# Performance work log

Measured on AMD Instinct MI355X. Metric: run time of the kernel, lower is better.

## Reference

```python
import jax, jax.numpy as jnp
import numpy as np

EMB_DIM = 1024
HEAD_SIZE = 128
B, T = 8, 2048


def setup_inputs() -> dict:
    key = jax.random.key(0)
    kx, kk, kq, kv = jax.random.split(key, 4)
    x = jax.random.normal(kx, (B, T, EMB_DIM), dtype=jnp.float32)
    # torch nn.Linear(emb_dim, head_size, bias=False): weight [head_size, emb_dim], y = x @ W.T
    # store transposed as [emb_dim, head_size] for direct matmul
    s = 1.0 / np.sqrt(EMB_DIM)
    Wk = jax.random.uniform(kk, (EMB_DIM, HEAD_SIZE), dtype=jnp.float32, minval=-s, maxval=s)
    Wq = jax.random.uniform(kq, (EMB_DIM, HEAD_SIZE), dtype=jnp.float32, minval=-s, maxval=s)
    Wv = jax.random.uniform(kv, (EMB_DIM, HEAD_SIZE), dtype=jnp.float32, minval=-s, maxval=s)
    return {"x": x, "Wk": Wk, "Wq": Wq, "Wv": Wv}


def reference(x, Wk, Wq, Wv):
    Bb, Tt, C = x.shape
    k = jnp.einsum('btc,ch->bth', x, Wk)
    q = jnp.einsum('btc,ch->bth', x, Wq)
    v = jnp.einsum('btc,ch->bth', x, Wv)
    # NOTE: original computes k @ q^T (not q @ k^T) and scales by C**-0.5 (C = emb_dim)
    wei = jnp.einsum('bih,bjh->bij', k, q) * (C ** -0.5)  # [B, T, T]
    causal = jnp.tril(jnp.ones((Tt, Tt), dtype=bool))
    wei = jnp.where(causal, wei, -jnp.inf)
    wei = jax.nn.softmax(wei, axis=-1)
    out = jnp.einsum('bij,bjh->bih', wei, v)  # [B, T, head_size]
    return out
```

## Files before the change

kernel.cpp:

```cpp
#include <hip/hip_runtime.h>
#include <hip/hip_bf16.h>
#include <stdint.h>

#define Bn 8
#define Tn 2048
#define Cn 1024
#define Hn 128

typedef __attribute__((ext_vector_type(8))) short short8;
typedef __attribute__((ext_vector_type(4))) short short4v;
typedef __attribute__((ext_vector_type(4))) float f32x4;
typedef __attribute__((ext_vector_type(4))) int int4v;

static __device__ __forceinline__ unsigned short f2bf(float f) {
    union { float f; unsigned int u; } v; v.f = f;
    return (unsigned short)((v.u + 0x7FFFu + ((v.u >> 16) & 1u)) >> 16);
}
static __device__ __forceinline__ float bf2f(unsigned short h) {
    union { unsigned int u; float f; } v; v.u = ((unsigned int)h) << 16;
    return v.f;
}

static __device__ __forceinline__ short8 cvt8(f32x4 a, f32x4 b) {
    union { unsigned int u[4]; short8 s; } r;
    asm("v_cvt_pk_bf16_f32 %0, %1, %2" : "=v"(r.u[0]) : "v"(a[0]), "v"(a[1]));
    asm("v_cvt_pk_bf16_f32 %0, %1, %2" : "=v"(r.u[1]) : "v"(a[2]), "v"(a[3]));
    asm("v_cvt_pk_bf16_f32 %0, %1, %2" : "=v"(r.u[2]) : "v"(b[0]), "v"(b[1]));
    asm("v_cvt_pk_bf16_f32 %0, %1, %2" : "=v"(r.u[3]) : "v"(b[2]), "v"(b[3]));
    return r.s;
}

static __device__ __forceinline__ void async16(const void* g, void* l) {
    __builtin_amdgcn_global_load_lds(
        (const __attribute__((address_space(1))) unsigned int*)g,
        (__attribute__((address_space(3))) unsigned int*)l,
        16, 0, 0);
}

#define KSCALE 0.04508422f

#define BASE_BYTES (3u * Bn * Tn * Hn * 2u + 3u * Hn * Cn * 2u)
#define SLOT_SH 2080
#define NBLK_FA 576
#define UPB_FA 72
#define CCHUNK 8

__global__ __launch_bounds__(256) void wt_prep(const float* __restrict__ Wk,
                                               const float* __restrict__ Wq,
                                               const float* __restrict__ Wv,
                                               unsigned short* __restrict__ WT) {
    int z = blockIdx.y;
    const float* W = (z == 0) ? Wk : (z == 1) ? Wq : Wv;
    unsigned short* wt = WT + (size_t)z * Hn * Cn;
    int o = blockIdx.x * 256 + threadIdx.x;
    int d = o >> 10;
    int k = o & (Cn - 1);
    wt[o] = f2bf(W[k * Hn + d]);
}

__global__ __launch_bounds__(512) void proj10(const float* __restrict__ x,
                                              const unsigned short* __restrict__ WTb,
                                              unsigned short* __restrict__ Kb,
                                              unsigned short* __restrict__ Qb,
                                              unsigned short* __restrict__ VT) {
    __shared__ __align__(16) unsigned short Bsm[2][384 * 64];
    __shared__ __align__(16) float Asm[2][64 * 64];
    int tid = threadIdx.x;
    int lane = tid & 63, w = tid >> 6;
    int lr = lane & 15, lg = lane >> 4;
    int wm = w >> 2, wn = w & 3;

    int u = ((int)(blockIdx.x & 7)) * 32 + ((int)blockIdx.x >> 3);
    int r0 = u * 64;

    const unsigned short* bsrcp[6];
    #pragma unroll
    for (int i = 0; i < 6; ++i) {
        int brow = (w * 6 + i) * 8 + (lane >> 3);
        int bslot = (lane & 7) ^ (brow & 7);
        bsrcp[i] = WTb + (size_t)brow * Cn + bslot * 8;
    }
    const float* asrcp[2];
    #pragma unroll
    for (int i = 0; i < 2; ++i) {
        int arow = (w * 2 + i) * 4 + (lane >> 4);
        int aslot = (lane & 15) ^ (arow & 7);
        asrcp[i] = x + (size_t)(r0 + arow) * Cn + aslot * 4;
    }

    auto STAGE = [&](int bb, int k0) {
        #pragma unroll
        for (int i = 0; i < 6; ++i)
            async16(bsrcp[i] + k0, &Bsm[bb][(w * 6 + i) * 512]);
        #pragma unroll
        for (int i = 0; i < 2; ++i)
            async16(asrcp[i] + k0, &Asm[bb][(w * 2 + i) * 256]);
    };

    f32x4 acc[2][6] = {};
    STAGE(0, 0);
    __syncthreads();
    int cur = 0;
    for (int ks = 0; ks < 16; ++ks) {
        if (ks < 15) STAGE(cur ^ 1, (ks + 1) * 64);
        const char* ab = (const char*)&Asm[cur][0];
        const char* bbp = (const char*)&Bsm[cur][0];
        #pragma unroll
        for (int kk = 0; kk < 2; ++kk) {
            short8 af[2], bf[6];
            #pragma unroll
            for (int m = 0; m < 2; ++m) {
                int row = wm * 32 + m * 16 + lr;
                const char* abase = ab + row * 256;
                f32x4 a0 = *(const f32x4*)(abase + (((kk * 8 + lg * 2)     ^ (row & 7)) << 4));
                f32x4 a1 = *(const f32x4*)(abase + (((kk * 8 + lg * 2 + 1) ^ (row & 7)) << 4));
                af[m] = cvt8(a0, a1);
            }
            #pragma unroll
            for (int c = 0; c < 6; ++c) {
                int row = wn * 96 + c * 16 + lr;
                bf[c] = *(const short8*)(bbp + row * 128 + (((kk * 4 + lg) ^ (row & 7)) << 4));
            }
            #pragma unroll
            for (int m = 0; m < 2; ++m)
                #pragma unroll
                for (int c = 0; c < 6; ++c)
                    acc[m][c] = __builtin_amdgcn_mfma_f32_16x16x32_bf16(af[m], bf[c], acc[m][c], 0, 0, 0);
        }
        __syncthreads();
        cur ^= 1;
    }

    int bb = r0 >> 11;
    int tb = r0 & 2047;
    #pragma unroll
    for (int m = 0; m < 2; ++m)
        #pragma unroll
        for (int c = 0; c < 6; ++c) {
            int col0 = wn * 96 + c * 16;
            int z = col0 >> 7;
            int d = (col0 & 127) + lr;
            if (z == 2) {
                int t = tb + wm * 32 + m * 16 + lg * 4;
                short4v pv;
                pv[0] = (short)f2bf(acc[m][c][0]);
                pv[1] = (short)f2bf(acc[m][c][1]);
                pv[2] = (short)f2bf(acc[m][c][2]);
                pv[3] = (short)f2bf(acc[m][c][3]);
                *(short4v*)(VT + ((size_t)(bb * Hn + d) << 11) + t) = pv;
            } else {
                unsigned short* outp = (z == 0) ? Kb : Qb;
                float sc = (z == 0) ? KSCALE : 1.0f;
                #pragma unroll
                for (int r = 0; r < 4; ++r) {
                    int i = r0 + wm * 32 + m * 16 + lg * 4 + r;
                    outp[(size_t)i * Hn + d] = f2bf(acc[m][c][r] * sc);
                }
            }
        }
}

__global__ __launch_bounds__(512) void fattn8(const unsigned short* __restrict__ Kb,
                                              const unsigned short* __restrict__ Qb,
                                              const unsigned short* __restrict__ VT,
                                              unsigned short* __restrict__ accP) {
    __shared__ __align__(16) unsigned short Ksm[2][32 * 128];
    __shared__ __align__(16) unsigned short Vsm[2][128 * 32];
    __shared__ __align__(16) unsigned short pbuf[8][16][48];
    int tid = threadIdx.x, lane = tid & 63, w = tid >> 6;
    int lr = lane & 15, lg = lane >> 4;

    int cpx = gridDim.x >> 3;
    int u = ((int)blockIdx.x & 7) * cpx + ((int)blockIdx.x >> 3);
    int b = u / UPB_FA, rem = u - b * UPB_FA;
    int g = 0, p = 0;
    for (;;) {
        int P = (4 * g + 4 + CCHUNK - 1) / CCHUNK;
        if (rem < P) { p = rem; break; }
        rem -= P; ++g;
    }
    int nt = 4 * g + 4;
    int P = (nt + CCHUNK - 1) / CCHUNK;
    int q = nt / P, r = nt % P;
    int begin = p * q + (p < r ? p : r);
    int size = q + (p < r ? 1 : 0);

    int i0 = g * 128 + w * 16;
    int tmax = (i0 + 15) >> 5;
    const unsigned short* kb = Kb + (size_t)b * Tn * Hn;
    const unsigned short* qb = Qb + (size_t)b * Tn * Hn;
    const unsigned short* vt = VT + (size_t)b * Hn * Tn;

    short8 kf[4];
    #pragma unroll
    for (int kk = 0; kk < 4; ++kk)
        kf[kk] = *(const short8*)(kb + (size_t)(i0 + lr) * Hn + kk * 32 + lg * 8);

    int krow = tid >> 4, kcol = (tid & 15) * 8;
    int vrow = tid >> 2, vcol = (tid & 3) * 8;
    int4v kreg, vreg;
    auto LOADT = [&](int tt) {
        int j0 = tt * 32;
        kreg = *(const int4v*)(qb + (size_t)(j0 + krow) * Hn + kcol);
        vreg = *(const int4v*)(vt + (size_t)vrow * Tn + j0 + vcol);
    };
    auto WRITET = [&](int bb) {
        *(int4v*)((char*)&Ksm[bb][0] + krow * 256 + ((kcol * 2) ^ ((krow & 7) << 4))) = kreg;
        *(int4v*)((char*)&Vsm[bb][0] + vrow * 64 + vcol * 2) = vreg;
    };

    f32x4 acc[8] = {};
    float ssum[4] = {0.f, 0.f, 0.f, 0.f};

    LOADT(begin);
    WRITET(0);
    __syncthreads();
    int cur = 0;
    for (int ti = 0; ti < size; ++ti) {
        int tt = begin + ti;
        if (ti + 1 < size) LOADT(tt + 1);
        if (tt <= tmax) {
            int j0 = tt * 32;
            const char* kbp = (const char*)&Ksm[cur][0];
            const char* vbp = (const char*)&Vsm[cur][0];
            f32x4 sa0 = {}, sa1 = {};
            #pragma unroll
            for (int kk = 0; kk < 4; ++kk) {
                int row = lr;
                short8 qf = *(const short8*)(kbp + row * 256 + (((kk * 64) + lg * 16) ^ ((row & 7) << 4)));
                sa0 = __builtin_amdgcn_mfma_f32_16x16x32_bf16(kf[kk], qf, sa0, 0, 0, 0);
            }
            #pragma unroll
            for (int kk = 0; kk < 4; ++kk) {
                int row = 16 + lr;
                short8 qf = *(const short8*)(kbp + row * 256 + (((kk * 64) + lg * 16) ^ ((row & 7) << 4)));
                sa1 = __builtin_amdgcn_mfma_f32_16x16x32_bf16(kf[kk], qf, sa1, 0, 0, 0);
            }
            bool needmask = (j0 + 31 > i0);
            #pragma unroll
            for (int rr = 0; rr < 4; ++rr) {
                float v0 = sa0[rr], v1 = sa1[rr];
                if (needmask) {
                    int i = i0 + lg * 4 + rr;
                    if (j0 + lr > i)      v0 = -1e30f;
                    if (j0 + 16 + lr > i) v1 = -1e30f;
                }
                float p0 = __builtin_amdgcn_exp2f(v0);
                float p1 = __builtin_amdgcn_exp2f(v1);
                ssum[rr] += p0 + p1;
                pbuf[w][lg * 4 + rr][lr] = f2bf(p0);
                pbuf[w][lg * 4 + rr][16 + lr] = f2bf(p1);
            }
            short8 pf = *(const short8*)(&pbuf[w][lr][lg * 8]);
            #pragma unroll
            for (int n = 0; n < 8; ++n) {
                int row = n * 16 + lr;
                short8 vf = *(const short8*)(vbp + row * 64 + lg * 16);
                acc[n] = __builtin_amdgcn_mfma_f32_16x16x32_bf16(pf, vf, acc[n], 0, 0, 0);
            }
        }
        if (ti + 1 < size) WRITET(cur ^ 1);
        __syncthreads();
        cur ^= 1;
    }

    unsigned short* dst = accP + (size_t)u * 8 * SLOT_SH + (size_t)w * SLOT_SH;
    #pragma unroll
    for (int n = 0; n < 8; ++n) {
        short4v pv;
        pv[0] = (short)f2bf(acc[n][0]);
        pv[1] = (short)f2bf(acc[n][1]);
        pv[2] = (short)f2bf(acc[n][2]);
        pv[3] = (short)f2bf(acc[n][3]);
        *(short4v*)(dst + n * 256 + lane * 4) = pv;
    }
    #pragma unroll
    for (int rr = 0; rr < 4; ++rr) {
        float s = ssum[rr];
        s += __shfl_xor(s, 1);
        s += __shfl_xor(s, 2);
        s += __shfl_xor(s, 4);
        s += __shfl_xor(s, 8);
        if (lr == 0) ((float*)(dst + 2048))[lg * 4 + rr] = s;
    }
}

__global__ __launch_bounds__(256) void combine3(const unsigned short* __restrict__ accP,
                                                float* __restrict__ out) {
    int cpx = gridDim.x >> 3;
    int bidx = ((int)blockIdx.x & 7) * cpx + ((int)blockIdx.x >> 3);
    int b = bidx >> 7, tile = bidx & 127;
    int g = tile >> 3, wq = tile & 7;
    int ub = b * UPB_FA;
    for (int gg = 0; gg < g; ++gg) ub += (4 * gg + 4 + CCHUNK - 1) / CCHUNK;
    int nt = 4 * g + 4;
    int P = (nt + CCHUNK - 1) / CCHUNK;

    int tid = threadIdx.x;
    int row = tid >> 4;
    int c8 = (tid & 15) * 8;

    const unsigned short* base = accP + ((size_t)ub * 8 + wq) * SLOT_SH;
    const size_t pstr = (size_t)8 * SLOT_SH;
    float den = 0.f;
    for (int pp = 0; pp < P; ++pp) den += ((const float*)(base + pp * pstr + 2048))[row];
    float inv = 1.0f / den;

    int lgg = row >> 2, r4 = row & 3;
    float ov[8];
    #pragma unroll
    for (int cc = 0; cc < 8; ++cc) {
        int col = c8 + cc;
        int n = col >> 4, lrr = col & 15;
        int flat = n * 256 + (lgg * 16 + lrr) * 4 + r4;
        float s = 0.f;
        for (int pp = 0; pp < P; ++pp) s += bf2f(base[pp * pstr + flat]);
        ov[cc] = s * inv;
    }
    float* op = out + ((size_t)(b * Tn + tile * 16 + row)) * Hn + c8;
    *(f32x4*)op       = f32x4{ov[0], ov[1], ov[2], ov[3]};
    *(f32x4*)(op + 4) = f32x4{ov[4], ov[5], ov[6], ov[7]};
}

__global__ __launch_bounds__(256) void attn(const unsigned short* __restrict__ Kb,
                                            const unsigned short* __restrict__ Qb,
                                            const unsigned short* __restrict__ VT,
                                            float* __restrict__ out) {
    __shared__ unsigned short pbuf[4][16][32];
    __shared__ __align__(16) float accbuf[4][16][132];
    __shared__ float ssbuf[4][16];
    int lane = threadIdx.x & 63;
    int w = threadIdx.x >> 6;
    int b = blockIdx.y;
    int xb = blockIdx.x;
    int tile = (xb & 1) ? (127 - (xb >> 1)) : (xb >> 1);
    int i0 = tile * 16;
    int lr = lane & 15, lg = lane >> 4;

    const unsigned short* kb = Kb + (size_t)b * Tn * Hn;
    const unsigned short* qb = Qb + (size_t)b * Tn * Hn;
    const unsigned short* vt = VT + (size_t)b * Hn * Tn;

    short8 kf[4];
    #pragma unroll
    for (int kk = 0; kk < 4; ++kk)
        kf[kk] = *(const short8*)(kb + (size_t)(i0 + lr) * Hn + kk * 32 + lg * 8);

    f32x4 acc[8] = {};
    float ssum[4] = {0.f, 0.f, 0.f, 0.f};

    int nt = (i0 + 15) / 32 + 1;
    for (int tt = w; tt < nt; tt += 4) {
        int j0 = tt * 32;
        f32x4 sa0 = {}, sa1 = {};
        #pragma unroll
        for (int kk = 0; kk < 4; ++kk) {
            short8 q0 = *(const short8*)(qb + (size_t)(j0 + lr) * Hn + kk * 32 + lg * 8);
            sa0 = __builtin_amdgcn_mfma_f32_16x16x32_bf16(kf[kk], q0, sa0, 0, 0, 0);
        }
        #pragma unroll
        for (int kk = 0; kk < 4; ++kk) {
            short8 q1 = *(const short8*)(qb + (size_t)(j0 + 16 + lr) * Hn + kk * 32 + lg * 8);
            sa1 = __builtin_amdgcn_mfma_f32_16x16x32_bf16(kf[kk], q1, sa1, 0, 0, 0);
        }
        bool needmask = (j0 + 31 > i0);
        #pragma unroll
        for (int r = 0; r < 4; ++r) {
            float v0 = sa0[r], v1 = sa1[r];
            if (needmask) {
                int i = i0 + lg * 4 + r;
                if (j0 + lr > i)      v0 = -1e30f;
                if (j0 + 16 + lr > i) v1 = -1e30f;
            }
            float p0 = __builtin_amdgcn_exp2f(v0);
            float p1 = __builtin_amdgcn_exp2f(v1);
            ssum[r] += p0 + p1;
            pbuf[w][lg * 4 + r][lr] = f2bf(p0);
            pbuf[w][lg * 4 + r][16 + lr] = f2bf(p1);
        }
        short8 pf = *(const short8*)(&pbuf[w][lr][lg * 8]);
        #pragma unroll
        for (int n = 0; n < 8; ++n) {
            short8 vf = *(const short8*)(vt + (size_t)(n * 16 + lr) * Tn + j0 + lg * 8);
            acc[n] = __builtin_amdgcn_mfma_f32_16x16x32_bf16(pf, vf, acc[n], 0, 0, 0);
        }
    }

    #pragma unroll
    for (int r = 0; r < 4; ++r) {
        float s = ssum[r];
        s += __shfl_xor(s, 1);
        s += __shfl_xor(s, 2);
        s += __shfl_xor(s, 4);
        s += __shfl_xor(s, 8);
        if (lr == 0) ssbuf[w][lg * 4 + r] = s;
    }
    #pragma unroll
    for (int n = 0; n < 8; ++n)
        #pragma unroll
        for (int r = 0; r < 4; ++r)
            accbuf[w][lg * 4 + r][n * 16 + lr] = acc[n][r];
    __syncthreads();

    int row = threadIdx.x >> 5;
    int col = (threadIdx.x & 31) * 4;
    #pragma unroll
    for (int h = 0; h < 2; ++h) {
        int rr = row + h * 8;
        f32x4 s = *(const f32x4*)(&accbuf[0][rr][col]);
        #pragma unroll
        for (int ww = 1; ww < 4; ++ww) {
            f32x4 t = *(const f32x4*)(&accbuf[ww][rr][col]);
            s[0] += t[0]; s[1] += t[1]; s[2] += t[2]; s[3] += t[3];
        }
        float den = ssbuf[0][rr] + ssbuf[1][rr] + ssbuf[2][rr] + ssbuf[3][rr];
        float inv = 1.0f / den;
        s[0] *= inv; s[1] *= inv; s[2] *= inv; s[3] *= inv;
        *(f32x4*)(&out[((size_t)(b * Tn + i0 + rr)) * Hn + col]) = s;
    }
}

extern "C" void kernel_launch(void* const* d_in, const int* in_sizes, int n_in,
                              void* d_out, int out_size, void* d_ws, size_t ws_size,
                              hipStream_t stream) {
    const float* x  = (const float*)d_in[0];
    const float* Wk = (const float*)d_in[1];
    const float* Wq = (const float*)d_in[2];
    const float* Wv = (const float*)d_in[3];

    unsigned short* Kb = (unsigned short*)d_ws;
    unsigned short* Qb = Kb + (size_t)Bn * Tn * Hn;
    unsigned short* VT = Qb + (size_t)Bn * Tn * Hn;
    unsigned short* WT = VT + (size_t)Bn * Tn * Hn;
    unsigned short* accP = (unsigned short*)((char*)d_ws + BASE_BYTES);

    wt_prep<<<dim3(512, 3), 256, 0, stream>>>(Wk, Wq, Wv, WT);
    proj10<<<dim3(256), 512, 0, stream>>>(x, WT, Kb, Qb, VT);

    const size_t need = (size_t)BASE_BYTES + (size_t)NBLK_FA * 8 * SLOT_SH * 2;
    if (ws_size >= need) {
        fattn8<<<dim3(NBLK_FA), 512, 0, stream>>>(Kb, Qb, VT, accP);
        combine3<<<dim3(1024), 256, 0, stream>>>(accP, (float*)d_out);
    } else {
        attn<<<dim3(128, 8), 256, 0, stream>>>(Kb, Qb, VT, (float*)d_out);
    }
}
```

Measured before the change: 85.87 us.

## Load projection A operand directly to registers with triple-buffered weight staging

The QKV projection kernel no longer stages the fp32 x tile through shared memory. Each lane loads its A fragment straight from global memory into double-buffered registers one step ahead. Weight tiles use a 3-deep shared-memory ring with a k-step of 32, and the loop waits on vmcnt counts instead of full syncthreads, with setprio around the MFMA block. This cuts LDS traffic and the shared-memory footprint and deepens prefetch, but it relies on hand-tuned waitcnt values and on uncoalesced direct global loads of x.

```diff
diff --git a/kernel.cpp b/kernel.cpp
--- a/kernel.cpp
+++ b/kernel.cpp
@@ -58,13 +58,12 @@
     wt[o] = f2bf(W[k * Hn + d]);
 }
 
-__global__ __launch_bounds__(512) void proj10(const float* __restrict__ x,
+__global__ __launch_bounds__(512) void proj11(const float* __restrict__ x,
                                               const unsigned short* __restrict__ WTb,
                                               unsigned short* __restrict__ Kb,
                                               unsigned short* __restrict__ Qb,
                                               unsigned short* __restrict__ VT) {
-    __shared__ __align__(16) unsigned short Bsm[2][384 * 64];
-    __shared__ __align__(16) float Asm[2][64 * 64];
+    __shared__ __align__(16) unsigned short Bsm[3][384 * 32];
     int tid = threadIdx.x;
     int lane = tid & 63, w = tid >> 6;
     int lr = lane & 15, lg = lane >> 4;
@@ -73,62 +72,70 @@
     int u = ((int)(blockIdx.x & 7)) * 32 + ((int)blockIdx.x >> 3);
     int r0 = u * 64;
 
-    const unsigned short* bsrcp[6];
-    #pragma unroll
-    for (int i = 0; i < 6; ++i) {
-        int brow = (w * 6 + i) * 8 + (lane >> 3);
-        int bslot = (lane & 7) ^ (brow & 7);
-        bsrcp[i] = WTb + (size_t)brow * Cn + bslot * 8;
-    }
-    const float* asrcp[2];
-    #pragma unroll
-    for (int i = 0; i < 2; ++i) {
-        int arow = (w * 2 + i) * 4 + (lane >> 4);
-        int aslot = (lane & 15) ^ (arow & 7);
-        asrcp[i] = x + (size_t)(r0 + arow) * Cn + aslot * 4;
-    }
-
+    const unsigned short* bsrc[3];
+    #pragma unroll
+    for (int i = 0; i < 3; ++i) {
+        int brow = (w * 3 + i) * 16 + (lane >> 2);
+        int bslot = (lane & 3) ^ ((brow >> 1) & 3);
+        bsrc[i] = WTb + (size_t)brow * Cn + bslot * 8;
+    }
     auto STAGE = [&](int bb, int k0) {
         #pragma unroll
-        for (int i = 0; i < 6; ++i)
-            async16(bsrcp[i] + k0, &Bsm[bb][(w * 6 + i) * 512]);
-        #pragma unroll
-        for (int i = 0; i < 2; ++i)
-            async16(asrcp[i] + k0, &Asm[bb][(w * 2 + i) * 256]);
+        for (int i = 0; i < 3; ++i)
+            async16(bsrc[i] + k0, &Bsm[bb][(w * 3 + i) * 512]);
     };
 
+    const float* aq0 = x + (size_t)(r0 + wm * 32 + lr) * Cn + lg * 8;
+    const float* aq1 = aq0 + 16 * Cn;
+    auto LOADA = [&](f32x4 (&d)[4], int k0) {
+        d[0] = *(const f32x4*)(aq0 + k0);
+        d[1] = *(const f32x4*)(aq0 + k0 + 4);
+        d[2] = *(const f32x4*)(aq1 + k0);
+        d[3] = *(const f32x4*)(aq1 + k0 + 4);
+    };
+
     f32x4 acc[2][6] = {};
+    f32x4 A0[4], A1[4];
+    int rbuf = 0;
+
     STAGE(0, 0);
-    __syncthreads();
-    int cur = 0;
-    for (int ks = 0; ks < 16; ++ks) {
-        if (ks < 15) STAGE(cur ^ 1, (ks + 1) * 64);
-        const char* ab = (const char*)&Asm[cur][0];
-        const char* bbp = (const char*)&Bsm[cur][0];
-        #pragma unroll
-        for (int kk = 0; kk < 2; ++kk) {
-            short8 af[2], bf[6];
-            #pragma unroll
-            for (int m = 0; m < 2; ++m) {
-                int row = wm * 32 + m * 16 + lr;
-                const char* abase = ab + row * 256;
-                f32x4 a0 = *(const f32x4*)(abase + (((kk * 8 + lg * 2)     ^ (row & 7)) << 4));
-                f32x4 a1 = *(const f32x4*)(abase + (((kk * 8 + lg * 2 + 1) ^ (row & 7)) << 4));
-                af[m] = cvt8(a0, a1);
-            }
-            #pragma unroll
-            for (int c = 0; c < 6; ++c) {
-                int row = wn * 96 + c * 16 + lr;
-                bf[c] = *(const short8*)(bbp + row * 128 + (((kk * 4 + lg) ^ (row & 7)) << 4));
-            }
-            #pragma unroll
-            for (int m = 0; m < 2; ++m)
-                #pragma unroll
-                for (int c = 0; c < 6; ++c)
-                    acc[m][c] = __builtin_amdgcn_mfma_f32_16x16x32_bf16(af[m], bf[c], acc[m][c], 0, 0, 0);
-        }
-        __syncthreads();
-        cur ^= 1;
+    STAGE(1, 32);
+    LOADA(A0, 0);
+
+    auto STEP = [&](int ks, f32x4 (&CUR)[4], f32x4 (&NXT)[4]) {
+        if (ks < 31) asm volatile("s_waitcnt vmcnt(7)" ::: "memory");
+        else         asm volatile("s_waitcnt vmcnt(0)" ::: "memory");
+        __builtin_amdgcn_s_barrier();
+        __builtin_amdgcn_sched_barrier(0);
+        if (ks + 2 < 32) {
+            int sb = rbuf + 2; if (sb >= 3) sb -= 3;
+            STAGE(sb, (ks + 2) * 32);
+        }
+        if (ks + 1 < 32) LOADA(NXT, (ks + 1) * 32);
+        __builtin_amdgcn_sched_barrier(0);
+        const char* bbp = (const char*)&Bsm[rbuf][0];
+        short8 af0 = cvt8(CUR[0], CUR[1]);
+        short8 af1 = cvt8(CUR[2], CUR[3]);
+        short8 bf[6];
+        #pragma unroll
+        for (int c = 0; c < 6; ++c) {
+            int row = wn * 96 + c * 16 + lr;
+            bf[c] = *(const short8*)(bbp + row * 64 + ((lg ^ ((row >> 1) & 3)) << 4));
+        }
+        __builtin_amdgcn_s_setprio(1);
+        #pragma unroll
+        for (int c = 0; c < 6; ++c) {
+            acc[0][c] = __builtin_amdgcn_mfma_f32_16x16x32_bf16(af0, bf[c], acc[0][c], 0, 0, 0);
+            acc[1][c] = __builtin_amdgcn_mfma_f32_16x16x32_bf16(af1, bf[c], acc[1][c], 0, 0, 0);
+        }
+        __builtin_amdgcn_s_setprio(0);
+        __builtin_amdgcn_sched_barrier(0);
+        ++rbuf; if (rbuf == 3) rbuf = 0;
+    };
+
+    for (int ks = 0; ks < 32; ks += 2) {
+        STEP(ks, A0, A1);
+        STEP(ks + 1, A1, A0);
     }
 
     int bb = r0 >> 11;
@@ -435,7 +442,7 @@
     unsigned short* accP = (unsigned short*)((char*)d_ws + BASE_BYTES);
 
     wt_prep<<<dim3(512, 3), 256, 0, stream>>>(Wk, Wq, Wv, WT);
-    proj10<<<dim3(256), 512, 0, stream>>>(x, WT, Kb, Qb, VT);
+    proj11<<<dim3(256), 512, 0, stream>>>(x, WT, Kb, Qb, VT);
 
     const size_t need = (size_t)BASE_BYTES + (size_t)NBLK_FA * 8 * SLOT_SH * 2;
     if (ws_size >= need) {
```

After: 104.5 us. 21.6% more time.

## Shrink projection GEMM tiles to 32 rows and 32-wide K steps with 512 blocks

Applied to the files above, without the earlier changes.

The QKV projection kernel now uses 32-row output tiles with 4 waves per block instead of 64-row tiles with 8 waves, and stages K in 32-element chunks with a new swizzle for the narrower LDS rows. The grid doubles to 512 blocks, halving LDS per block, which is meant to spread work over more CUs and raise occupancy. The cost is twice as many weight reloads per output row, twice the K-loop iterations and barriers, and less reuse of each loaded weight tile.

```diff
diff --git a/kernel.cpp b/kernel.cpp
--- a/kernel.cpp
+++ b/kernel.cpp
@@ -58,75 +58,66 @@
     wt[o] = f2bf(W[k * Hn + d]);
 }
 
-__global__ __launch_bounds__(512) void proj10(const float* __restrict__ x,
+__global__ __launch_bounds__(256) void proj12(const float* __restrict__ x,
                                               const unsigned short* __restrict__ WTb,
                                               unsigned short* __restrict__ Kb,
                                               unsigned short* __restrict__ Qb,
                                               unsigned short* __restrict__ VT) {
-    __shared__ __align__(16) unsigned short Bsm[2][384 * 64];
-    __shared__ __align__(16) float Asm[2][64 * 64];
+    __shared__ __align__(16) unsigned short Bsm[2][384 * 32];
+    __shared__ __align__(16) float Asm[2][32 * 32];
     int tid = threadIdx.x;
     int lane = tid & 63, w = tid >> 6;
     int lr = lane & 15, lg = lane >> 4;
-    int wm = w >> 2, wn = w & 3;
-
-    int u = ((int)(blockIdx.x & 7)) * 32 + ((int)blockIdx.x >> 3);
-    int r0 = u * 64;
-
-    const unsigned short* bsrcp[6];
+    int wn = w;
+
+    int u = ((int)(blockIdx.x & 7)) * 64 + ((int)blockIdx.x >> 3);
+    int r0 = u * 32;
+
+    const unsigned short* bsrc[6];
     #pragma unroll
     for (int i = 0; i < 6; ++i) {
-        int brow = (w * 6 + i) * 8 + (lane >> 3);
-        int bslot = (lane & 7) ^ (brow & 7);
-        bsrcp[i] = WTb + (size_t)brow * Cn + bslot * 8;
-    }
-    const float* asrcp[2];
-    #pragma unroll
-    for (int i = 0; i < 2; ++i) {
-        int arow = (w * 2 + i) * 4 + (lane >> 4);
-        int aslot = (lane & 15) ^ (arow & 7);
-        asrcp[i] = x + (size_t)(r0 + arow) * Cn + aslot * 4;
-    }
+        int brow = (w * 6 + i) * 16 + (lane >> 2);
+        int bslot = (lane & 3) ^ ((brow >> 1) & 3);
+        bsrc[i] = WTb + (size_t)brow * Cn + bslot * 8;
+    }
+    int arow = w * 8 + (lane >> 3);
+    int aslot = (lane & 7) ^ (arow & 7);
+    const float* asrc = x + (size_t)(r0 + arow) * Cn + aslot * 4;
 
     auto STAGE = [&](int bb, int k0) {
         #pragma unroll
         for (int i = 0; i < 6; ++i)
-            async16(bsrcp[i] + k0, &Bsm[bb][(w * 6 + i) * 512]);
-        #pragma unroll
-        for (int i = 0; i < 2; ++i)
-            async16(asrcp[i] + k0, &Asm[bb][(w * 2 + i) * 256]);
+            async16(bsrc[i] + k0, &Bsm[bb][(w * 6 + i) * 512]);
+        async16(asrc + k0, &Asm[bb][w * 256]);
     };
 
     f32x4 acc[2][6] = {};
     STAGE(0, 0);
     __syncthreads();
     int cur = 0;
-    for (int ks = 0; ks < 16; ++ks) {
-        if (ks < 15) STAGE(cur ^ 1, (ks + 1) * 64);
+    for (int ks = 0; ks < 32; ++ks) {
+        if (ks < 31) STAGE(cur ^ 1, (ks + 1) * 32);
         const char* ab = (const char*)&Asm[cur][0];
         const char* bbp = (const char*)&Bsm[cur][0];
-        #pragma unroll
-        for (int kk = 0; kk < 2; ++kk) {
-            short8 af[2], bf[6];
+        short8 af[2], bf[6];
+        #pragma unroll
+        for (int m = 0; m < 2; ++m) {
+            int row = m * 16 + lr;
+            const char* abase = ab + row * 128;
+            f32x4 a0 = *(const f32x4*)(abase + (((lg * 2)     ^ (row & 7)) << 4));
+            f32x4 a1 = *(const f32x4*)(abase + (((lg * 2 + 1) ^ (row & 7)) << 4));
+            af[m] = cvt8(a0, a1);
+        }
+        #pragma unroll
+        for (int c = 0; c < 6; ++c) {
+            int row = wn * 96 + c * 16 + lr;
+            bf[c] = *(const short8*)(bbp + row * 64 + ((lg ^ ((row >> 1) & 3)) << 4));
+        }
+        #pragma unroll
+        for (int m = 0; m < 2; ++m)
             #pragma unroll
-            for (int m = 0; m < 2; ++m) {
-                int row = wm * 32 + m * 16 + lr;
-                const char* abase = ab + row * 256;
-                f32x4 a0 = *(const f32x4*)(abase + (((kk * 8 + lg * 2)     ^ (row & 7)) << 4));
-                f32x4 a1 = *(const f32x4*)(abase + (((kk * 8 + lg * 2 + 1) ^ (row & 7)) << 4));
-                af[m] = cvt8(a0, a1);
-            }
-            #pragma unroll
-            for (int c = 0; c < 6; ++c) {
-                int row = wn * 96 + c * 16 + lr;
-                bf[c] = *(const short8*)(bbp + row * 128 + (((kk * 4 + lg) ^ (row & 7)) << 4));
-            }
-            #pragma unroll
-            for (int m = 0; m < 2; ++m)
-                #pragma unroll
-                for (int c = 0; c < 6; ++c)
-                    acc[m][c] = __builtin_amdgcn_mfma_f32_16x16x32_bf16(af[m], bf[c], acc[m][c], 0, 0, 0);
-        }
+            for (int c = 0; c < 6; ++c)
+                acc[m][c] = __builtin_amdgcn_mfma_f32_16x16x32_bf16(af[m], bf[c], acc[m][c], 0, 0, 0);
         __syncthreads();
         cur ^= 1;
     }
@@ -141,7 +132,7 @@
             int z = col0 >> 7;
             int d = (col0 & 127) + lr;
             if (z == 2) {
-                int t = tb + wm * 32 + m * 16 + lg * 4;
+                int t = tb + m * 16 + lg * 4;
                 short4v pv;
                 pv[0] = (short)f2bf(acc[m][c][0]);
                 pv[1] = (short)f2bf(acc[m][c][1]);
@@ -153,7 +144,7 @@
                 float sc = (z == 0) ? KSCALE : 1.0f;
                 #pragma unroll
                 for (int r = 0; r < 4; ++r) {
-                    int i = r0 + wm * 32 + m * 16 + lg * 4 + r;
+                    int i = r0 + m * 16 + lg * 4 + r;
                     outp[(size_t)i * Hn + d] = f2bf(acc[m][c][r] * sc);
                 }
             }
@@ -435,7 +426,7 @@
     unsigned short* accP = (unsigned short*)((char*)d_ws + BASE_BYTES);
 
     wt_prep<<<dim3(512, 3), 256, 0, stream>>>(Wk, Wq, Wv, WT);
-    proj10<<<dim3(256), 512, 0, stream>>>(x, WT, Kb, Qb, VT);
+    proj12<<<dim3(512), 256, 0, stream>>>(x, WT, Kb, Qb, VT);
 
     const size_t need = (size_t)BASE_BYTES + (size_t)NBLK_FA * 8 * SLOT_SH * 2;
     if (ws_size >= need) {
```

Result: slower. 92.75 us (+8.0%).
